# Performance work log

Measured on AMD Instinct MI355X. Metric: run time of the kernel, lower is better.

## Reference

```python
import jax, jax.numpy as jnp
import numpy as np

S, B, D, F, E, K = 1024, 2, 512, 2048, 8, 2


def setup_inputs() -> dict:
    key = jax.random.key(0)
    ks = jax.random.split(key, 12)
    s = lambda *sh: 1.0 / np.sqrt(sh[0])
    inp = {
        "x": jax.random.normal(ks[0], (S, B, D), dtype=jnp.float32),
        # gate: nn.Linear(d_model, n_experts)
        "Wg": jax.random.normal(ks[1], (D, E), dtype=jnp.float32) * s(D),
        "bg": jnp.zeros((E,), dtype=jnp.float32),
        # routed experts: stacked FFN params (E copies of expert)
        "W1": jax.random.normal(ks[2], (E, D, F), dtype=jnp.float32) * s(D),
        "b1": jnp.zeros((E, F), dtype=jnp.float32),
        "W2": jax.random.normal(ks[3], (E, F, D), dtype=jnp.float32) * s(F),
        "b2": jnp.zeros((E, D), dtype=jnp.float32),
        # shared expert (single FFN)
        "Ws1": jax.random.normal(ks[4], (D, F), dtype=jnp.float32) * s(D),
        "bs1": jnp.zeros((F,), dtype=jnp.float32),
        "Ws2": jax.random.normal(ks[5], (F, D), dtype=jnp.float32) * s(F),
        "bs2": jnp.zeros((D,), dtype=jnp.float32),
    }
    return inp


def reference(x, Wg, bg, W1, b1, W2, b2, Ws1, bs1, Ws2, bs2):
    # gate_logits: (S, B, E)
    gate_logits = jnp.einsum("sbd,de->sbe", x, Wg) + bg
    # top-k per token (eval mode: k = n_experts_per_token, t = 1.0)
    weights, selected = jax.lax.top_k(gate_logits, K)  # (S,B,K)
    weights = jax.nn.softmax(weights.astype(jnp.float32), axis=-1)
    # combine weights per expert: (S,B,E)
    onehot = jax.nn.one_hot(selected, E, dtype=weights.dtype)  # (S,B,K,E)
    comb = jnp.einsum("sbk,sbke->sbe", weights, onehot)
    # routed experts computed densely, combined with per-token routing weight
    h = jax.nn.relu(jnp.einsum("sbd,edf->sbef", x, W1) + b1)  # (S,B,E,F)
    y = jnp.einsum("sbef,efd->sbed", h, W2) + b2              # (S,B,E,D)
    out = jnp.einsum("sbe,sbed->sbd", comb, y)
    # shared expert, scaled by 1/k
    hs = jax.nn.relu(jnp.einsum("sbd,df->sbf", x, Ws1) + bs1)
    shared = jnp.einsum("sbf,fd->sbd", hs, Ws2) + bs2
    out = out + (1.0 / K) * shared
    return out
```

## Files before the change

### kernel.cpp

```cpp
#include <hip/hip_runtime.h>
#include <hip/hip_bf16.h>
#include <stdint.h>

#define TT 2048
#define DD 512
#define FF 2048
#define EE 8

typedef unsigned short u16;
typedef __attribute__((ext_vector_type(8))) unsigned short ushort8v;
typedef __attribute__((ext_vector_type(8))) short short8;
typedef __attribute__((ext_vector_type(4))) float float4v;

__device__ __forceinline__ u16 f2bf(float f) {
    unsigned u = __float_as_uint(f);
    u += 0x7FFF + ((u >> 16) & 1);
    return (u16)(u >> 16);
}

__device__ __forceinline__ void gl_lds16(const u16* g, u16* l) {
    __builtin_amdgcn_global_load_lds(
        (const __attribute__((address_space(1))) unsigned int*)g,
        (__attribute__((address_space(3))) unsigned int*)l, 16, 0, 0);
}

#define WS_HB   0ull
#define WS_XG   (WS_HB + 6144ull*2048*2)
#define WS_WT1  (WS_XG + 2048ull*512*2)
#define WS_ME   (WS_WT1 + 9ull*2048*512*2)
#define WS_MW   (WS_ME + 16384)
#define WS_RT   (WS_MW + 16384)
#define WS_WROW (WS_RT + 16384)
#define WS_TROW (WS_WROW + 16384)
#define WS_RTG  (WS_TROW + 16384)
#define WS_WT2  (WS_RTG + 128)
#define WS_YB   (WS_WT2 + 9ull*2048*512*2)
#define YS      (6144ull*512)
#define WS_NEED (WS_YB + 2ull*6144*512*4)

__device__ __forceinline__ void conv_unit(int j, const float* __restrict__ srcE,
                                          const float* __restrict__ srcS,
                                          u16* __restrict__ dst,
                                          int R, int C, int shC, u16* Ls) {
    int mid = j >> 8, t2 = j & 255;
    int tr = t2 >> shC, tc = t2 & ((1 << shC) - 1);
    int r0 = tr * 64, c0 = tc * 64;
    const float* src = (mid < 8) ? srcE + (size_t)mid * R * C : srcS;
    u16* dstm = dst + (size_t)mid * R * C;
    int t = threadIdx.x;
#pragma unroll
    for (int i = 0; i < 4; ++i) {
        int rr = (t >> 4) + i * 16;
        int cc = (t & 15) * 4;
        float4v v = *(const float4v*)(src + (size_t)(r0 + rr) * C + c0 + cc);
#pragma unroll
        for (int jx = 0; jx < 4; ++jx) Ls[(cc + jx) * 72 + rr] = f2bf(v[jx]);
    }
    __syncthreads();
#pragma unroll
    for (int jj = 0; jj < 2; ++jj) {
        int slot = t + jj * 256;
        int cc = slot >> 3, r8 = (slot & 7) * 8;
        ushort8v o = *(const ushort8v*)&Ls[cc * 72 + r8];
        *(ushort8v*)(dstm + (size_t)(c0 + cc) * R + r0 + r8) = o;
    }
}

__device__ __forceinline__ void gate_wave(int t, int lane,
                                          const float* __restrict__ x,
                                          const float* __restrict__ Wg,
                                          const float* __restrict__ bg,
                                          int* __restrict__ metaE,
                                          float* __restrict__ metaW,
                                          u16* __restrict__ xg) {
    const float* xp = x + (size_t)t * DD + lane * 8;
    float4v x0 = *(const float4v*)xp;
    float4v x1 = *(const float4v*)(xp + 4);
    float xf[8] = {x0[0], x0[1], x0[2], x0[3], x1[0], x1[1], x1[2], x1[3]};
    float acc[EE] = {0.f, 0.f, 0.f, 0.f, 0.f, 0.f, 0.f, 0.f};
#pragma unroll
    for (int g = 0; g < 8; ++g) {
        const float* wp = Wg + (size_t)(lane * 8 + g) * EE;
        float4v w0 = *(const float4v*)wp;
        float4v w1 = *(const float4v*)(wp + 4);
        acc[0] += xf[g] * w0[0]; acc[1] += xf[g] * w0[1];
        acc[2] += xf[g] * w0[2]; acc[3] += xf[g] * w0[3];
        acc[4] += xf[g] * w1[0]; acc[5] += xf[g] * w1[1];
        acc[6] += xf[g] * w1[2]; acc[7] += xf[g] * w1[3];
    }
#pragma unroll
    for (int off = 1; off < 64; off <<= 1) {
#pragma unroll
        for (int e = 0; e < EE; ++e) acc[e] += __shfl_xor(acc[e], off, 64);
    }
    ushort8v xv;
#pragma unroll
    for (int jx = 0; jx < 4; ++jx) xv[jx] = f2bf(x0[jx]);
#pragma unroll
    for (int jx = 0; jx < 4; ++jx) xv[4 + jx] = f2bf(x1[jx]);
    *(ushort8v*)(xg + (size_t)t * DD + lane * 8) = xv;
    if (lane == 0) {
#pragma unroll
        for (int e = 0; e < EE; ++e) acc[e] += bg[e];
        int e0 = 0; float l0 = acc[0];
#pragma unroll
        for (int e = 1; e < EE; ++e) if (acc[e] > l0) { l0 = acc[e]; e0 = e; }
        int e1 = -1; float l1 = -3.4e38f;
#pragma unroll
        for (int e = 0; e < EE; ++e)
            if (e != e0 && acc[e] > l1) { l1 = acc[e]; e1 = e; }
        float ex = __expf(l1 - l0);
        float w0 = 1.f / (1.f + ex);
        metaE[2 * t] = e0; metaE[2 * t + 1] = e1;
        metaW[2 * t] = w0; metaW[2 * t + 1] = 1.f - w0;
    }
}

__global__ __launch_bounds__(256) void fused1_k(
    const float* __restrict__ x, const float* __restrict__ Wg,
    const float* __restrict__ bg,
    const float* __restrict__ W1, const float* __restrict__ Ws1,
    const float* __restrict__ W2, const float* __restrict__ Ws2,
    float* __restrict__ out, u16* __restrict__ xg,
    u16* __restrict__ Wt1, u16* __restrict__ Wt2,
    int* __restrict__ metaE, float* __restrict__ metaW, int nconv) {
    __shared__ __align__(16) u16 Ls[64 * 72];
    int b = blockIdx.x, tid = threadIdx.x;
    if (b < nconv) {
        if (b < 2304) conv_unit(b, W1, Ws1, Wt1, DD, FF, 5, Ls);
        else          conv_unit(b - 2304, W2, Ws2, Wt2, FF, DD, 3, Ls);
    } else if (b < nconv + 512) {
        int gb = b - nconv;
        gate_wave(gb * 4 + (tid >> 6), tid & 63, x, Wg, bg, metaE, metaW, xg);
    } else {
        int zb = b - nconv - 512;
        float* op = out + (size_t)zb * 8192;
#pragma unroll
        for (int it = 0; it < 8; ++it)
            *(float4v*)(op + it * 1024 + tid * 4) = (float4v){0.f, 0.f, 0.f, 0.f};
    }
}

__global__ __launch_bounds__(256) void conv2_k(const float* __restrict__ W2,
                                               const float* __restrict__ Ws2,
                                               u16* __restrict__ Wt2) {
    __shared__ __align__(16) u16 Ls[64 * 72];
    conv_unit(blockIdx.x, W2, Ws2, Wt2, FF, DD, 3, Ls);
}

__global__ __launch_bounds__(256) void rank_k(const int* __restrict__ metaE,
                                              const float* __restrict__ metaW,
                                              int* __restrict__ routing,
                                              int* __restrict__ rtok,
                                              float* __restrict__ wrow,
                                              int* __restrict__ trow) {
    __shared__ __align__(16) char smem[16384];
    u16* er      = (u16*)smem;
    int* segCnt  = (int*)(smem + 8192);
    int* segBase = (int*)(smem + 10240);
    int* expTot  = (int*)(smem + 12288);
    int tid = threadIdx.x, wv = tid >> 6, lane = tid & 63;
    unsigned long long below = (lane == 0) ? 0ull : ((~0ull) >> (64 - lane));
    for (int s = wv * 16; s < wv * 16 + 16; ++s) {
        int entry = s * 64 + lane;
        int e = metaE[entry];
        int rk = 0;
#pragma unroll
        for (int ee = 0; ee < 8; ++ee) {
            unsigned long long m = __ballot(e == ee);
            if (e == ee) rk = __popcll(m & below);
            if (lane == ee) segCnt[s * 8 + ee] = __popcll(m);
        }
        er[entry] = (u16)(e | (rk << 4));
    }
    __syncthreads();
    if (tid < 8) {
        int s = 0;
        for (int g = 0; g < 64; ++g) { segBase[g * 8 + tid] = s; s += segCnt[g * 8 + tid]; }
        expTot[tid] = s;
    }
    __syncthreads();
    if (tid == 0) {
        int s = 0;
        for (int e = 0; e < 8; ++e) { int c = expTot[e]; expTot[8 + e] = s; s += c; }
    }
    __syncthreads();
    if (tid < 8) { routing[tid] = expTot[8 + tid]; routing[8 + tid] = expTot[tid]; }
    for (int i = 0; i < 16; ++i) {
        int entry = tid + i * 256;
        int v = er[entry];
        int e = v & 15, rk = v >> 4;
        int row = expTot[8 + e] + segBase[(entry >> 6) * 8 + e] + rk;
        rtok[row] = entry >> 1;
        wrow[row] = metaW[entry];
        trow[entry] = row;
    }
}

__global__ __launch_bounds__(256) void gemmA_k(
    const u16* __restrict__ xg, const u16* __restrict__ Wt1,
    const float* __restrict__ b1, const float* __restrict__ bs1,
    const int* __restrict__ routing, const int* __restrict__ rtok,
    u16* __restrict__ hbuf) {
    __shared__ __align__(16) u16 As[2][128 * 64];
    __shared__ __align__(16) u16 Bs[2][128 * 64];
    const int* offs = routing; const int* cnt = routing + 8;
    int j = blockIdx.x, tid = threadIdx.x;
    int rt, ct, Mloc, hRowBase, rowBase; bool routed;
    const u16* Bsrc; const float* bias;
    if (j < 256) {
        rt = j >> 4; ct = j & 15; Mloc = 128; rowBase = rt * 128;
        Bsrc = Wt1 + (size_t)8 * FF * DD; bias = bs1;
        hRowBase = 4096 + rt * 128; routed = false;
    } else {
        int jr = j - 256; int e = jr & 7; int rc = jr >> 3;
        rt = rc >> 4; ct = rc & 15;
        int M = cnt[e]; if (rt * 128 >= M) return;
        Mloc = M - rt * 128; if (Mloc > 128) Mloc = 128;
        rowBase = offs[e] + rt * 128;
        Bsrc = Wt1 + (size_t)e * FF * DD; bias = b1 + e * FF;
        hRowBase = rowBase; routed = true;
    }
    int n0 = ct * 128;
    int lane = tid & 63, w = tid >> 6, ln = lane & 15, quad = lane >> 4;
    int wm = w >> 1, wn = w & 1;
    int lr8 = lane >> 3;
    int cs = (lane & 7) ^ lr8;
    const u16* ApS[4];
#pragma unroll
    for (int i = 0; i < 4; ++i) {
        int r = w * 32 + i * 8 + lr8;
        int tok;
        if (routed) { int br = rowBase + r; if (br > 4095) br = 4095; tok = rtok[br]; }
        else tok = rowBase + r;
        ApS[i] = xg + (size_t)tok * DD + cs * 8;
    }
    const u16* BpS[4];
#pragma unroll
    for (int i = 0; i < 4; ++i) {
        int r = w * 32 + i * 8 + lr8;
        BpS[i] = Bsrc + (size_t)(n0 + r) * DD + cs * 8;
    }
    float4v acc[4][4];
#pragma unroll
    for (int a = 0; a < 4; ++a)
#pragma unroll
        for (int b = 0; b < 4; ++b) acc[a][b] = (float4v){0.f, 0.f, 0.f, 0.f};

    auto stage = [&](int kt, int pb) {
#pragma unroll
        for (int i = 0; i < 4; ++i)
            gl_lds16(ApS[i] + kt * 64, &As[pb][0] + (w * 32 + i * 8) * 64);
#pragma unroll
        for (int i = 0; i < 4; ++i)
            gl_lds16(BpS[i] + kt * 64, &Bs[pb][0] + (w * 32 + i * 8) * 64);
    };

    stage(0, 0);
#pragma unroll
    for (int kt = 0; kt < 8; ++kt) {
        int pb = kt & 1;
        if (kt < 7) {
            stage(kt + 1, pb ^ 1);
            asm volatile("s_waitcnt vmcnt(8)" ::: "memory");
        } else {
            asm volatile("s_waitcnt vmcnt(0)" ::: "memory");
        }
        __builtin_amdgcn_s_barrier();
        __builtin_amdgcn_sched_barrier(0);
        const u16* Ab = &As[pb][0]; const u16* Bb = &Bs[pb][0];
#pragma unroll
        for (int s = 0; s < 2; ++s) {
            int chs = ((s * 4 + quad) ^ (ln & 7)) * 8;
            short8 Af[4], Bf[4];
#pragma unroll
            for (int a = 0; a < 4; ++a) {
                int ra = wm * 64 + a * 16 + ln;
                Af[a] = *(const short8*)(Ab + ra * 64 + chs);
            }
#pragma unroll
            for (int b = 0; b < 4; ++b) {
                int rb = wn * 64 + b * 16 + ln;
                Bf[b] = *(const short8*)(Bb + rb * 64 + chs);
            }
#pragma unroll
            for (int a = 0; a < 4; ++a)
#pragma unroll
                for (int b = 0; b < 4; ++b)
                    acc[a][b] = __builtin_amdgcn_mfma_f32_16x16x32_bf16(Af[a], Bf[b], acc[a][b], 0, 0, 0);
        }
        __builtin_amdgcn_sched_barrier(0);
        __builtin_amdgcn_s_barrier();
    }
#pragma unroll
    for (int b = 0; b < 4; ++b) {
        int n = n0 + wn * 64 + b * 16 + ln;
        float bv = bias[n];
#pragma unroll
        for (int a = 0; a < 4; ++a) {
#pragma unroll
            for (int i = 0; i < 4; ++i) {
                int lr = wm * 64 + a * 16 + quad * 4 + i;
                if (lr < Mloc) {
                    float v = acc[a][b][i] + bv;
                    v = v > 0.f ? v : 0.f;
                    hbuf[(size_t)(hRowBase + lr) * FF + n] = f2bf(v);
                }
            }
        }
    }
}

__global__ __launch_bounds__(256) void gemmB_k(
    const u16* __restrict__ hbuf, const u16* __restrict__ Wt2,
    const float* __restrict__ b2, const float* __restrict__ bs2,
    const int* __restrict__ routing, float* __restrict__ ybuf) {
    __shared__ __align__(16) u16 As[2][128 * 64];
    __shared__ __align__(16) u16 Bs[2][128 * 64];
    const int* offs = routing; const int* cnt = routing + 8;
    int j = blockIdx.x, tid = threadIdx.x;
    int rt, ct, ks, Mloc, aRowBase;
    const u16* Bsrc; const float* bias;
    if (j < 128) {
        ks = j & 1; ct = (j >> 1) & 3; rt = j >> 3;
        Mloc = 128; aRowBase = 4096 + rt * 128;
        Bsrc = Wt2 + (size_t)8 * DD * FF; bias = bs2;
    } else {
        int jr = j - 128; int e = jr & 7; int rc = jr >> 3;
        ks = rc & 1; ct = (rc >> 1) & 3; rt = rc >> 3;
        int M = cnt[e]; if (rt * 128 >= M) return;
        Mloc = M - rt * 128; if (Mloc > 128) Mloc = 128;
        aRowBase = offs[e] + rt * 128;
        Bsrc = Wt2 + (size_t)e * DD * FF; bias = b2 + e * DD;
    }
    int n0 = ct * 128;
    int lane = tid & 63, w = tid >> 6, ln = lane & 15, quad = lane >> 4;
    int wm = w >> 1, wn = w & 1;
    int lr8 = lane >> 3;
    int cs = (lane & 7) ^ lr8;
    const u16* ApS[4];
#pragma unroll
    for (int i = 0; i < 4; ++i) {
        int r = w * 32 + i * 8 + lr8;
        ApS[i] = hbuf + (size_t)(aRowBase + r) * FF + ks * 1024 + cs * 8;
    }
    const u16* BpS[4];
#pragma unroll
    for (int i = 0; i < 4; ++i) {
        int r = w * 32 + i * 8 + lr8;
        BpS[i] = Bsrc + (size_t)(n0 + r) * FF + ks * 1024 + cs * 8;
    }
    float4v acc[4][4];
#pragma unroll
    for (int a = 0; a < 4; ++a)
#pragma unroll
        for (int b = 0; b < 4; ++b) acc[a][b] = (float4v){0.f, 0.f, 0.f, 0.f};

    auto stage = [&](int kt, int pb) {
#pragma unroll
        for (int i = 0; i < 4; ++i)
            gl_lds16(ApS[i] + kt * 64, &As[pb][0] + (w * 32 + i * 8) * 64);
#pragma unroll
        for (int i = 0; i < 4; ++i)
            gl_lds16(BpS[i] + kt * 64, &Bs[pb][0] + (w * 32 + i * 8) * 64);
    };

    stage(0, 0);
#pragma unroll
    for (int kt = 0; kt < 16; ++kt) {
        int pb = kt & 1;
        if (kt < 15) {
            stage(kt + 1, pb ^ 1);
            asm volatile("s_waitcnt vmcnt(8)" ::: "memory");
        } else {
            asm volatile("s_waitcnt vmcnt(0)" ::: "memory");
        }
        __builtin_amdgcn_s_barrier();
        __builtin_amdgcn_sched_barrier(0);
        const u16* Ab = &As[pb][0]; const u16* Bb = &Bs[pb][0];
#pragma unroll
        for (int s = 0; s < 2; ++s) {
            int chs = ((s * 4 + quad) ^ (ln & 7)) * 8;
            short8 Af[4], Bf[4];
#pragma unroll
            for (int a = 0; a < 4; ++a) {
                int ra = wm * 64 + a * 16 + ln;
                Af[a] = *(const short8*)(Ab + ra * 64 + chs);
            }
#pragma unroll
            for (int b = 0; b < 4; ++b) {
                int rb = wn * 64 + b * 16 + ln;
                Bf[b] = *(const short8*)(Bb + rb * 64 + chs);
            }
#pragma unroll
            for (int a = 0; a < 4; ++a)
#pragma unroll
                for (int b = 0; b < 4; ++b)
                    acc[a][b] = __builtin_amdgcn_mfma_f32_16x16x32_bf16(Af[a], Bf[b], acc[a][b], 0, 0, 0);
        }
        __builtin_amdgcn_sched_barrier(0);
        __builtin_amdgcn_s_barrier();
    }
    float* yb = ybuf + (size_t)ks * YS;
#pragma unroll
    for (int b = 0; b < 4; ++b) {
        int n = n0 + wn * 64 + b * 16 + ln;
        float bv = (ks == 0) ? bias[n] : 0.f;
#pragma unroll
        for (int a = 0; a < 4; ++a) {
#pragma unroll
            for (int i = 0; i < 4; ++i) {
                int lr = wm * 64 + a * 16 + quad * 4 + i;
                if (lr < Mloc)
                    yb[(size_t)(aRowBase + lr) * DD + n] = acc[a][b][i] + bv;
            }
        }
    }
}

__global__ __launch_bounds__(256) void combine_k(
    const float* __restrict__ ybuf, const int* __restrict__ trow,
    const float* __restrict__ metaW, float* __restrict__ out) {
    int tid = threadIdx.x;
    int tok = blockIdx.x * 2 + (tid >> 7);
    int q = (tid & 127) * 4;
    int r0 = trow[2 * tok], r1 = trow[2 * tok + 1];
    float w0 = metaW[2 * tok], w1 = metaW[2 * tok + 1];
    const float* ya = ybuf;
    const float* yb = ybuf + YS;
    float4v y0a = *(const float4v*)(ya + (size_t)r0 * DD + q);
    float4v y0b = *(const float4v*)(yb + (size_t)r0 * DD + q);
    float4v y1a = *(const float4v*)(ya + (size_t)r1 * DD + q);
    float4v y1b = *(const float4v*)(yb + (size_t)r1 * DD + q);
    float4v ysa = *(const float4v*)(ya + (size_t)(4096 + tok) * DD + q);
    float4v ysb = *(const float4v*)(yb + (size_t)(4096 + tok) * DD + q);
    float4v o;
#pragma unroll
    for (int i = 0; i < 4; ++i)
        o[i] = w0 * (y0a[i] + y0b[i]) + w1 * (y1a[i] + y1b[i]) + 0.5f * (ysa[i] + ysb[i]);
    *(float4v*)(out + (size_t)tok * DD + q) = o;
}

__global__ __launch_bounds__(256) void gemmBat_k(
    const u16* __restrict__ hbuf, const u16* __restrict__ Wt2,
    const float* __restrict__ b2, const float* __restrict__ bs2,
    const int* __restrict__ routing, const int* __restrict__ rtok,
    const float* __restrict__ wrow, float* __restrict__ out) {
    __shared__ __align__(16) u16 As[2][64 * 64];
    __shared__ __align__(16) u16 Bs[2][128 * 64];
    const int* offs = routing; const int* cnt = routing + 8;
    int j = blockIdx.x, tid = threadIdx.x;
    int rt, ct, ks, Mloc, aRowBase; bool sh;
    const u16* Bsrc; const float* bias;
    if (j < 256) {
        sh = true; rt = j >> 3; int sub = j & 7; ct = sub >> 1; ks = sub & 1;
        Mloc = 64; aRowBase = 4096 + rt * 64;
        Bsrc = Wt2 + (size_t)8 * DD * FF; bias = bs2;
    } else {
        sh = false; int jr = j - 256; int e = jr & 7; int rc = jr >> 3;
        rt = rc >> 3; ct = (rc >> 1) & 3; ks = rc & 1;
        int M = cnt[e]; if (rt * 64 >= M) return;
        Mloc = M - rt * 64; if (Mloc > 64) Mloc = 64;
        aRowBase = offs[e] + rt * 64;
        Bsrc = Wt2 + (size_t)e * DD * FF; bias = b2 + e * DD;
    }
    int n0 = ct * 128;
    int lane = tid & 63, w = tid >> 6, ln = lane & 15, quad = lane >> 4;
    int lr8 = lane >> 3;
    int cs = (lane & 7) ^ lr8;
    const u16* ApS[2];
#pragma unroll
    for (int i = 0; i < 2; ++i) {
        int r = w * 16 + i * 8 + lr8;
        ApS[i] = hbuf + (size_t)(aRowBase + r) * FF + ks * 1024 + cs * 8;
    }
    const u16* BpS[4];
#pragma unroll
    for (int i = 0; i < 4; ++i) {
        int r = w * 32 + i * 8 + lr8;
        BpS[i] = Bsrc + (size_t)(n0 + r) * FF + ks * 1024 + cs * 8;
    }
    float4v acc[2][4];
#pragma unroll
    for (int a = 0; a < 2; ++a)
#pragma unroll
        for (int b = 0; b < 4; ++b) acc[a][b] = (float4v){0.f, 0.f, 0.f, 0.f};
    auto stage = [&](int kt, int pb) {
        u16* Ab = &As[pb][0]; u16* Bb = &Bs[pb][0];
#pragma unroll
        for (int i = 0; i < 2; ++i)
            gl_lds16(ApS[i] + kt * 64, Ab + (w * 16 + i * 8) * 64);
#pragma unroll
        for (int i = 0; i < 4; ++i)
            gl_lds16(BpS[i] + kt * 64, Bb + (w * 32 + i * 8) * 64);
    };
    stage(0, 0);
#pragma unroll
    for (int kt = 0; kt < 16; ++kt) {
        int pb = kt & 1;
        if (kt < 15) {
            stage(kt + 1, pb ^ 1);
            asm volatile("s_waitcnt vmcnt(6)" ::: "memory");
        } else {
            asm volatile("s_waitcnt vmcnt(0)" ::: "memory");
        }
        __builtin_amdgcn_s_barrier();
        __builtin_amdgcn_sched_barrier(0);
        const u16* Ab = &As[pb][0]; const u16* Bb = &Bs[pb][0];
#pragma unroll
        for (int s = 0; s < 2; ++s) {
            int chs = ((s * 4 + quad) ^ (ln & 7)) * 8;
            short8 Af[2], Bf[4];
#pragma unroll
            for (int a = 0; a < 2; ++a) {
                int ra = (w & 1) * 32 + a * 16 + ln;
                Af[a] = *(const short8*)(Ab + ra * 64 + chs);
            }
#pragma unroll
            for (int b = 0; b < 4; ++b) {
                int rb = (w >> 1) * 64 + b * 16 + ln;
                Bf[b] = *(const short8*)(Bb + rb * 64 + chs);
            }
#pragma unroll
            for (int a = 0; a < 2; ++a)
#pragma unroll
                for (int b = 0; b < 4; ++b)
                    acc[a][b] = __builtin_amdgcn_mfma_f32_16x16x32_bf16(Af[a], Bf[b], acc[a][b], 0, 0, 0);
        }
        __builtin_amdgcn_sched_barrier(0);
        __builtin_amdgcn_s_barrier();
    }
    float bv[4];
#pragma unroll
    for (int b = 0; b < 4; ++b)
        bv[b] = (ks == 0) ? bias[n0 + (w >> 1) * 64 + b * 16 + ln] : 0.f;
#pragma unroll
    for (int a = 0; a < 2; ++a) {
#pragma unroll
        for (int i = 0; i < 4; ++i) {
            int lr = (w & 1) * 32 + a * 16 + quad * 4 + i;
            if (lr < Mloc) {
                int row = aRowBase + lr;
                int t; float wr;
                if (sh) { t = row - 4096; wr = 0.5f; }
                else    { t = rtok[row]; wr = wrow[row]; }
                float* op = out + (size_t)t * DD;
#pragma unroll
                for (int b = 0; b < 4; ++b) {
                    int n = n0 + (w >> 1) * 64 + b * 16 + ln;
                    atomicAdd(op + n, wr * (acc[a][b][i] + bv[b]));
                }
            }
        }
    }
}

extern "C" void kernel_launch(void* const* d_in, const int* in_sizes, int n_in,
                              void* d_out, int out_size, void* d_ws, size_t ws_size,
                              hipStream_t stream) {
    const float* x   = (const float*)d_in[0];
    const float* Wg  = (const float*)d_in[1];
    const float* bg  = (const float*)d_in[2];
    const float* W1  = (const float*)d_in[3];
    const float* b1  = (const float*)d_in[4];
    const float* W2  = (const float*)d_in[5];
    const float* b2  = (const float*)d_in[6];
    const float* Ws1 = (const float*)d_in[7];
    const float* bs1 = (const float*)d_in[8];
    const float* Ws2 = (const float*)d_in[9];
    const float* bs2 = (const float*)d_in[10];
    float* out = (float*)d_out;

    char* ws = (char*)d_ws;
    u16*   hbuf    = (u16*)(ws + WS_HB);
    u16*   xg      = (u16*)(ws + WS_XG);
    u16*   Wt1     = (u16*)(ws + WS_WT1);
    int*   metaE   = (int*)(ws + WS_ME);
    float* metaW   = (float*)(ws + WS_MW);
    int*   rtok    = (int*)(ws + WS_RT);
    float* wrow    = (float*)(ws + WS_WROW);
    int*   trow    = (int*)(ws + WS_TROW);
    int*   routing = (int*)(ws + WS_RTG);
    bool   big     = ws_size >= WS_NEED;
    u16*   Wt2     = big ? (u16*)(ws + WS_WT2) : Wt1;
    float* ybuf    = (float*)(ws + WS_YB);
    int    nconv   = big ? 4608 : 2304;
    int    ngrid1  = big ? (nconv + 512) : (nconv + 640);

    fused1_k<<<ngrid1, 256, 0, stream>>>(x, Wg, bg, W1, Ws1, W2, Ws2,
                                         out, xg, Wt1, Wt2, metaE, metaW, nconv);
    rank_k<<<1, 256, 0, stream>>>(metaE, metaW, routing, rtok, wrow, trow);
    gemmA_k<<<4352, 256, 0, stream>>>(xg, Wt1, b1, bs1, routing, rtok, hbuf);
    if (big) {
        gemmB_k<<<2176, 256, 0, stream>>>(hbuf, Wt2, b2, bs2, routing, ybuf);
        combine_k<<<1024, 256, 0, stream>>>(ybuf, trow, metaW, out);
    } else {
        conv2_k<<<2304, 256, 0, stream>>>(W2, Ws2, Wt2);
        gemmBat_k<<<4352, 256, 0, stream>>>(hbuf, Wt2, b2, bs2, routing, rtok, wrow, out);
    }
}
```

Before: 215.1 us.

## Halve GEMM M-tiles, drop LDS double buffering, move W2 conversion into gemmA

Both expert GEMM kernels now use 64-row M tiles instead of 128, which doubles the block count and reduces padding waste on partially filled expert tiles. Double-buffered LDS staging is replaced by a single buffer with a full vmcnt wait each K step. Part of the W2/Ws2 bf16 conversion moves out of fused1_k into extra gemmA blocks so it can overlap with the first GEMM. The trade-offs are the loss of load/compute overlap inside a block and lower MFMA reuse per A/B fragment.

After: 208.6 us. 3.0% less time.

```diff
diff --git a/kernel.cpp b/kernel.cpp
--- a/kernel.cpp
+++ b/kernel.cpp
@@ -201,23 +201,28 @@
     const u16* __restrict__ xg, const u16* __restrict__ Wt1,
     const float* __restrict__ b1, const float* __restrict__ bs1,
     const int* __restrict__ routing, const int* __restrict__ rtok,
-    u16* __restrict__ hbuf) {
-    __shared__ __align__(16) u16 As[2][128 * 64];
-    __shared__ __align__(16) u16 Bs[2][128 * 64];
+    u16* __restrict__ hbuf,
+    const float* __restrict__ W2, const float* __restrict__ Ws2,
+    u16* __restrict__ Wt2, int ncv) {
+    __shared__ __align__(16) u16 SM[12288];
+    int j = blockIdx.x, tid = threadIdx.x;
+    if (j < ncv) { conv_unit(j, W2, Ws2, Wt2, FF, DD, 3, SM); return; }
+    j -= ncv;
+    u16* As = SM;
+    u16* Bs = SM + 4096;
     const int* offs = routing; const int* cnt = routing + 8;
-    int j = blockIdx.x, tid = threadIdx.x;
     int rt, ct, Mloc, hRowBase, rowBase; bool routed;
     const u16* Bsrc; const float* bias;
-    if (j < 256) {
-        rt = j >> 4; ct = j & 15; Mloc = 128; rowBase = rt * 128;
+    if (j < 512) {
+        rt = j >> 4; ct = j & 15; Mloc = 64; rowBase = rt * 64;
         Bsrc = Wt1 + (size_t)8 * FF * DD; bias = bs1;
-        hRowBase = 4096 + rt * 128; routed = false;
+        hRowBase = 4096 + rt * 64; routed = false;
     } else {
-        int jr = j - 256; int e = jr & 7; int rc = jr >> 3;
+        int jr = j - 512; int e = jr & 7; int rc = jr >> 3;
         rt = rc >> 4; ct = rc & 15;
-        int M = cnt[e]; if (rt * 128 >= M) return;
-        Mloc = M - rt * 128; if (Mloc > 128) Mloc = 128;
-        rowBase = offs[e] + rt * 128;
+        int M = cnt[e]; if (rt * 64 >= M) return;
+        Mloc = M - rt * 64; if (Mloc > 64) Mloc = 64;
+        rowBase = offs[e] + rt * 64;
         Bsrc = Wt1 + (size_t)e * FF * DD; bias = b1 + e * FF;
         hRowBase = rowBase; routed = true;
     }
@@ -226,10 +231,10 @@
     int wm = w >> 1, wn = w & 1;
     int lr8 = lane >> 3;
     int cs = (lane & 7) ^ lr8;
-    const u16* ApS[4];
-#pragma unroll
-    for (int i = 0; i < 4; ++i) {
-        int r = w * 32 + i * 8 + lr8;
+    const u16* ApS[2];
+#pragma unroll
+    for (int i = 0; i < 2; ++i) {
+        int r = w * 16 + i * 8 + lr8;
         int tok;
         if (routed) { int br = rowBase + r; if (br > 4095) br = 4095; tok = rtok[br]; }
         else tok = rowBase + r;
@@ -241,55 +246,42 @@
         int r = w * 32 + i * 8 + lr8;
         BpS[i] = Bsrc + (size_t)(n0 + r) * DD + cs * 8;
     }
-    float4v acc[4][4];
-#pragma unroll
-    for (int a = 0; a < 4; ++a)
+    float4v acc[2][4];
+#pragma unroll
+    for (int a = 0; a < 2; ++a)
 #pragma unroll
         for (int b = 0; b < 4; ++b) acc[a][b] = (float4v){0.f, 0.f, 0.f, 0.f};
 
-    auto stage = [&](int kt, int pb) {
+#pragma unroll
+    for (int kt = 0; kt < 8; ++kt) {
+#pragma unroll
+        for (int i = 0; i < 2; ++i)
+            gl_lds16(ApS[i] + kt * 64, As + (w * 16 + i * 8) * 64);
 #pragma unroll
         for (int i = 0; i < 4; ++i)
-            gl_lds16(ApS[i] + kt * 64, &As[pb][0] + (w * 32 + i * 8) * 64);
-#pragma unroll
-        for (int i = 0; i < 4; ++i)
-            gl_lds16(BpS[i] + kt * 64, &Bs[pb][0] + (w * 32 + i * 8) * 64);
-    };
-
-    stage(0, 0);
-#pragma unroll
-    for (int kt = 0; kt < 8; ++kt) {
-        int pb = kt & 1;
-        if (kt < 7) {
-            stage(kt + 1, pb ^ 1);
-            asm volatile("s_waitcnt vmcnt(8)" ::: "memory");
-        } else {
-            asm volatile("s_waitcnt vmcnt(0)" ::: "memory");
-        }
+            gl_lds16(BpS[i] + kt * 64, Bs + (w * 32 + i * 8) * 64);
+        asm volatile("s_waitcnt vmcnt(0)" ::: "memory");
         __builtin_amdgcn_s_barrier();
-        __builtin_amdgcn_sched_barrier(0);
-        const u16* Ab = &As[pb][0]; const u16* Bb = &Bs[pb][0];
 #pragma unroll
         for (int s = 0; s < 2; ++s) {
             int chs = ((s * 4 + quad) ^ (ln & 7)) * 8;
-            short8 Af[4], Bf[4];
-#pragma unroll
-            for (int a = 0; a < 4; ++a) {
-                int ra = wm * 64 + a * 16 + ln;
-                Af[a] = *(const short8*)(Ab + ra * 64 + chs);
+            short8 Af[2], Bf[4];
+#pragma unroll
+            for (int a = 0; a < 2; ++a) {
+                int ra = wm * 32 + a * 16 + ln;
+                Af[a] = *(const short8*)(As + ra * 64 + chs);
             }
 #pragma unroll
             for (int b = 0; b < 4; ++b) {
                 int rb = wn * 64 + b * 16 + ln;
-                Bf[b] = *(const short8*)(Bb + rb * 64 + chs);
-            }
-#pragma unroll
-            for (int a = 0; a < 4; ++a)
+                Bf[b] = *(const short8*)(Bs + rb * 64 + chs);
+            }
+#pragma unroll
+            for (int a = 0; a < 2; ++a)
 #pragma unroll
                 for (int b = 0; b < 4; ++b)
                     acc[a][b] = __builtin_amdgcn_mfma_f32_16x16x32_bf16(Af[a], Bf[b], acc[a][b], 0, 0, 0);
         }
-        __builtin_amdgcn_sched_barrier(0);
         __builtin_amdgcn_s_barrier();
     }
 #pragma unroll
@@ -297,10 +289,10 @@
         int n = n0 + wn * 64 + b * 16 + ln;
         float bv = bias[n];
 #pragma unroll
-        for (int a = 0; a < 4; ++a) {
+        for (int a = 0; a < 2; ++a) {
 #pragma unroll
             for (int i = 0; i < 4; ++i) {
-                int lr = wm * 64 + a * 16 + quad * 4 + i;
+                int lr = wm * 32 + a * 16 + quad * 4 + i;
                 if (lr < Mloc) {
                     float v = acc[a][b][i] + bv;
                     v = v > 0.f ? v : 0.f;
@@ -315,22 +307,23 @@
     const u16* __restrict__ hbuf, const u16* __restrict__ Wt2,
     const float* __restrict__ b2, const float* __restrict__ bs2,
     const int* __restrict__ routing, float* __restrict__ ybuf) {
-    __shared__ __align__(16) u16 As[2][128 * 64];
-    __shared__ __align__(16) u16 Bs[2][128 * 64];
+    __shared__ __align__(16) u16 SM[12288];
+    u16* As = SM;
+    u16* Bs = SM + 4096;
     const int* offs = routing; const int* cnt = routing + 8;
     int j = blockIdx.x, tid = threadIdx.x;
     int rt, ct, ks, Mloc, aRowBase;
     const u16* Bsrc; const float* bias;
-    if (j < 128) {
-        ks = j & 1; ct = (j >> 1) & 3; rt = j >> 3;
-        Mloc = 128; aRowBase = 4096 + rt * 128;
+    if (j < 256) {
+        rt = j >> 3; ct = (j >> 1) & 3; ks = j & 1;
+        Mloc = 64; aRowBase = 4096 + rt * 64;
         Bsrc = Wt2 + (size_t)8 * DD * FF; bias = bs2;
     } else {
-        int jr = j - 128; int e = jr & 7; int rc = jr >> 3;
+        int jr = j - 256; int e = jr & 7; int rc = jr >> 3;
         ks = rc & 1; ct = (rc >> 1) & 3; rt = rc >> 3;
-        int M = cnt[e]; if (rt * 128 >= M) return;
-        Mloc = M - rt * 128; if (Mloc > 128) Mloc = 128;
-        aRowBase = offs[e] + rt * 128;
+        int M = cnt[e]; if (rt * 64 >= M) return;
+        Mloc = M - rt * 64; if (Mloc > 64) Mloc = 64;
+        aRowBase = offs[e] + rt * 64;
         Bsrc = Wt2 + (size_t)e * DD * FF; bias = b2 + e * DD;
     }
     int n0 = ct * 128;
@@ -338,10 +331,10 @@
     int wm = w >> 1, wn = w & 1;
     int lr8 = lane >> 3;
     int cs = (lane & 7) ^ lr8;
-    const u16* ApS[4];
-#pragma unroll
-    for (int i = 0; i < 4; ++i) {
-        int r = w * 32 + i * 8 + lr8;
+    const u16* ApS[2];
+#pragma unroll
+    for (int i = 0; i < 2; ++i) {
+        int r = w * 16 + i * 8 + lr8;
         ApS[i] = hbuf + (size_t)(aRowBase + r) * FF + ks * 1024 + cs * 8;
     }
     const u16* BpS[4];
@@ -350,55 +343,42 @@
         int r = w * 32 + i * 8 + lr8;
         BpS[i] = Bsrc + (size_t)(n0 + r) * FF + ks * 1024 + cs * 8;
     }
-    float4v acc[4][4];
-#pragma unroll
-    for (int a = 0; a < 4; ++a)
+    float4v acc[2][4];
+#pragma unroll
+    for (int a = 0; a < 2; ++a)
 #pragma unroll
         for (int b = 0; b < 4; ++b) acc[a][b] = (float4v){0.f, 0.f, 0.f, 0.f};
 
-    auto stage = [&](int kt, int pb) {
+#pragma unroll
+    for (int kt = 0; kt < 16; ++kt) {
+#pragma unroll
+        for (int i = 0; i < 2; ++i)
+            gl_lds16(ApS[i] + kt * 64, As + (w * 16 + i * 8) * 64);
 #pragma unroll
         for (int i = 0; i < 4; ++i)
-            gl_lds16(ApS[i] + kt * 64, &As[pb][0] + (w * 32 + i * 8) * 64);
-#pragma unroll
-        for (int i = 0; i < 4; ++i)
-            gl_lds16(BpS[i] + kt * 64, &Bs[pb][0] + (w * 32 + i * 8) * 64);
-    };
-
-    stage(0, 0);
-#pragma unroll
-    for (int kt = 0; kt < 16; ++kt) {
-        int pb = kt & 1;
-        if (kt < 15) {
-            stage(kt + 1, pb ^ 1);
-            asm volatile("s_waitcnt vmcnt(8)" ::: "memory");
-        } else {
-            asm volatile("s_waitcnt vmcnt(0)" ::: "memory");
-        }
+            gl_lds16(BpS[i] + kt * 64, Bs + (w * 32 + i * 8) * 64);
+        asm volatile("s_waitcnt vmcnt(0)" ::: "memory");
         __builtin_amdgcn_s_barrier();
-        __builtin_amdgcn_sched_barrier(0);
-        const u16* Ab = &As[pb][0]; const u16* Bb = &Bs[pb][0];
 #pragma unroll
         for (int s = 0; s < 2; ++s) {
             int chs = ((s * 4 + quad) ^ (ln & 7)) * 8;
-            short8 Af[4], Bf[4];
-#pragma unroll
-            for (int a = 0; a < 4; ++a) {
-                int ra = wm * 64 + a * 16 + ln;
-                Af[a] = *(const short8*)(Ab + ra * 64 + chs);
+            short8 Af[2], Bf[4];
+#pragma unroll
+            for (int a = 0; a < 2; ++a) {
+                int ra = wm * 32 + a * 16 + ln;
+                Af[a] = *(const short8*)(As + ra * 64 + chs);
             }
 #pragma unroll
             for (int b = 0; b < 4; ++b) {
                 int rb = wn * 64 + b * 16 + ln;
-                Bf[b] = *(const short8*)(Bb + rb * 64 + chs);
-            }
-#pragma unroll
-            for (int a = 0; a < 4; ++a)
+                Bf[b] = *(const short8*)(Bs + rb * 64 + chs);
+            }
+#pragma unroll
+            for (int a = 0; a < 2; ++a)
 #pragma unroll
                 for (int b = 0; b < 4; ++b)
                     acc[a][b] = __builtin_amdgcn_mfma_f32_16x16x32_bf16(Af[a], Bf[b], acc[a][b], 0, 0, 0);
         }
-        __builtin_amdgcn_sched_barrier(0);
         __builtin_amdgcn_s_barrier();
     }
     float* yb = ybuf + (size_t)ks * YS;
@@ -407,10 +387,10 @@
         int n = n0 + wn * 64 + b * 16 + ln;
         float bv = (ks == 0) ? bias[n] : 0.f;
 #pragma unroll
-        for (int a = 0; a < 4; ++a) {
+        for (int a = 0; a < 2; ++a) {
 #pragma unroll
             for (int i = 0; i < 4; ++i) {
-                int lr = wm * 64 + a * 16 + quad * 4 + i;
+                int lr = wm * 32 + a * 16 + quad * 4 + i;
                 if (lr < Mloc)
                     yb[(size_t)(aRowBase + lr) * DD + n] = acc[a][b][i] + bv;
             }
@@ -584,17 +564,21 @@
     bool   big     = ws_size >= WS_NEED;
     u16*   Wt2     = big ? (u16*)(ws + WS_WT2) : Wt1;
     float* ybuf    = (float*)(ws + WS_YB);
-    int    nconv   = big ? 4608 : 2304;
-    int    ngrid1  = big ? (nconv + 512) : (nconv + 640);
-
-    fused1_k<<<ngrid1, 256, 0, stream>>>(x, Wg, bg, W1, Ws1, W2, Ws2,
-                                         out, xg, Wt1, Wt2, metaE, metaW, nconv);
-    rank_k<<<1, 256, 0, stream>>>(metaE, metaW, routing, rtok, wrow, trow);
-    gemmA_k<<<4352, 256, 0, stream>>>(xg, Wt1, b1, bs1, routing, rtok, hbuf);
+
     if (big) {
-        gemmB_k<<<2176, 256, 0, stream>>>(hbuf, Wt2, b2, bs2, routing, ybuf);
+        fused1_k<<<2816, 256, 0, stream>>>(x, Wg, bg, W1, Ws1, W2, Ws2,
+                                           out, xg, Wt1, Wt2, metaE, metaW, 2304);
+        rank_k<<<1, 256, 0, stream>>>(metaE, metaW, routing, rtok, wrow, trow);
+        gemmA_k<<<2304 + 512 + 8192, 256, 0, stream>>>(
+            xg, Wt1, b1, bs1, routing, rtok, hbuf, W2, Ws2, Wt2, 2304);
+        gemmB_k<<<256 + 4096, 256, 0, stream>>>(hbuf, Wt2, b2, bs2, routing, ybuf);
         combine_k<<<1024, 256, 0, stream>>>(ybuf, trow, metaW, out);
     } else {
+        fused1_k<<<2944, 256, 0, stream>>>(x, Wg, bg, W1, Ws1, W2, Ws2,
+                                           out, xg, Wt1, Wt2, metaE, metaW, 2304);
+        rank_k<<<1, 256, 0, stream>>>(metaE, metaW, routing, rtok, wrow, trow);
+        gemmA_k<<<512 + 8192, 256, 0, stream>>>(
+            xg, Wt1, b1, bs1, routing, rtok, hbuf, W2, Ws2, Wt2, 0);
         conv2_k<<<2304, 256, 0, stream>>>(W2, Ws2, Wt2);
         gemmBat_k<<<4352, 256, 0, stream>>>(hbuf, Wt2, b2, bs2, routing, rtok, wrow, out);
     }
```
